# Kernel tuning notes

Hardware: AMD Instinct MI355X
Metric: run time of the kernel (lower is better)

The kernel has to match this reference:

```python
import jax, jax.numpy as jnp
import numpy as np

HEADS = 8
IH, IW = 32, 32
C_IN, C_OUT = 512, 512


def setup_inputs() -> dict:
    key = jax.random.key(0)
    k1, k2, k3, k4, k5 = jax.random.split(key, 5)
    B = 32
    n = IH + IW + (IH // 2) * (IW // 2)  # pooled kv length = 320
    x = jax.random.normal(k1, (B, C_IN, IH, IW), dtype=jnp.float32)
    # 1x1 conv weights stored as [out, in] (bias-free qkv, biased output proj)
    Wqkv = jax.random.normal(k2, (3 * C_IN, C_IN), dtype=jnp.float32) * 0.02
    Wout = jax.random.normal(k3, (C_OUT, C_IN), dtype=jnp.float32) * 0.02
    bout = jnp.zeros((C_OUT,), dtype=jnp.float32)
    pos_embed = jax.random.normal(k4, (1, IH * IW, n), dtype=jnp.float32) * 0.2
    return {"x": x, "Wqkv": Wqkv, "Wout": Wout, "bout": bout, "pos_embed": pos_embed}


def _pool_gate(t, B, C, H, W):
    # adaptive_avg_pool2d(.,(None,1)) == mean over width -> [B,C,H]
    th = t.mean(axis=3)
    # adaptive_avg_pool2d(.,(1,None)) (+permute) == mean over height -> [B,C,W]
    tw = t.mean(axis=2)
    # adaptive_avg_pool2d to (H//2, W//2) with even dims == 2x2 average pooling
    tp = t.reshape(B, C, H // 2, 2, W // 2, 2).mean(axis=(3, 5)).reshape(B, C, -1)
    s = jax.nn.sigmoid(jnp.concatenate([th, tw, tp], axis=2))  # [B,C,n]
    d = C // HEADS
    # 'b (h d) n -> b h n d'
    return s.reshape(B, HEADS, d, -1).transpose(0, 1, 3, 2)


def reference(x, Wqkv, Wout, bout, pos_embed):
    B, C, H, W = x.shape
    d = C // HEADS
    scale = d ** (-0.5)
    qkv = jnp.einsum('bchw,oc->bohw', x, Wqkv)  # 1x1 conv, no bias
    q, k, v = jnp.split(qkv, 3, axis=1)
    # 'b (h d) ih iw -> b h (ih iw) d'
    q = q.reshape(B, HEADS, d, H * W).transpose(0, 1, 3, 2)
    k = _pool_gate(k, B, C, H, W)  # [B,h,n,d]
    v = _pool_gate(v, B, C, H, W)  # [B,h,n,d]
    dots = jnp.einsum('bhsd,bhnd->bhsn', q, k) * scale + pos_embed  # pos_embed [1,s,n] broadcasts
    attn = jax.nn.softmax(dots, axis=-1)
    out = jnp.einsum('bhsn,bhnd->bhsd', attn, v)
    # 'b h (ih iw) d -> b (h d) ih iw'
    out = out.transpose(0, 1, 3, 2).reshape(B, HEADS * d, H, W)
    out = jnp.einsum('bchw,oc->bohw', out, Wout) + bout[None, :, None, None]
    return out
```

## Files before the change

kernel.cpp:

```cpp
#include <hip/hip_runtime.h>
#include <hip/hip_bf16.h>
#include <math.h>

#define HEADS 8
#define CH    512
#define S     1024
#define NKV   320
#define DH    64
#define BATCH 32

typedef __attribute__((ext_vector_type(8))) short short8;
typedef __attribute__((ext_vector_type(4))) short short4v;
typedef __attribute__((ext_vector_type(4))) float float4v;
typedef __attribute__((ext_vector_type(4))) unsigned int uint4v;

__device__ __forceinline__ short f2bf(float f) {
    __hip_bfloat16 h = __float2bfloat16(f);
    return *reinterpret_cast<short*>(&h);
}

__device__ __forceinline__ float fexp2(float x) {
#if __has_builtin(__builtin_amdgcn_exp2f)
    return __builtin_amdgcn_exp2f(x);
#else
    return exp2f(x);
#endif
}

#define GLOAD_LDS16(gp, lp) __builtin_amdgcn_global_load_lds( \
    (const __attribute__((address_space(1))) void*)(gp),      \
    (__attribute__((address_space(3))) void*)(lp), 16, 0, 0)

__global__ __launch_bounds__(256) void pool_kernel2(const float* __restrict__ x,
                                                    short* __restrict__ xpT) {
    __shared__ float sm[4][1024];
    __shared__ short smT[320 * 34];
    const int w = threadIdx.x >> 6;
    const int l = threadIdx.x & 63;
    const int b = blockIdx.y, c0 = blockIdx.x * 32;
    for (int it = 0; it < 8; ++it) {
        const int cix = it * 4 + w;
        const float* src = x + ((size_t)b * 512 + c0 + cix) * 1024;
        #pragma unroll
        for (int j = 0; j < 16; ++j) sm[w][j * 64 + l] = src[j * 64 + l];
        const float* pl = sm[w];
        #pragma unroll
        for (int g = 0; g < 5; ++g) {
            const int nn = g * 64 + l;
            float r;
            if (nn < 32) {
                const int h = nn; float s = 0.f;
                #pragma unroll
                for (int ww = 0; ww < 32; ++ww) s += pl[h * 32 + ww];
                r = s * (1.0f / 32.0f);
            } else if (nn < 64) {
                const int ww = nn - 32; float s = 0.f;
                #pragma unroll
                for (int h = 0; h < 32; ++h) s += pl[h * 32 + ww];
                r = s * (1.0f / 32.0f);
            } else {
                const int i = nn - 64;
                const int ph = i >> 4, pw = i & 15;
                r = 0.25f * (pl[(2 * ph) * 32 + 2 * pw]     + pl[(2 * ph) * 32 + 2 * pw + 1] +
                             pl[(2 * ph + 1) * 32 + 2 * pw] + pl[(2 * ph + 1) * 32 + 2 * pw + 1]);
            }
            smT[nn * 34 + cix] = f2bf(r);
        }
    }
    __syncthreads();
    short* dst = xpT + (size_t)b * NKV * 512 + c0;
    const int r0 = threadIdx.x >> 4, dwi = threadIdx.x & 15;
    #pragma unroll
    for (int pass = 0; pass < 20; ++pass) {
        const int r = pass * 16 + r0;
        const unsigned int v =
            (unsigned int)(unsigned short)smT[r * 34 + dwi * 2] |
            ((unsigned int)(unsigned short)smT[r * 34 + dwi * 2 + 1] << 16);
        *(unsigned int*)&dst[(size_t)r * 512 + dwi * 2] = v;
    }
}

__global__ __launch_bounds__(256) void tcast(const float* __restrict__ in,
                                             short* __restrict__ out, int R, int C) {
    __shared__ float sm[64][65];
    const int t = threadIdx.x;
    const int c0 = blockIdx.x * 64, r0 = blockIdx.y * 64;
    const float* ib = in + ((size_t)blockIdx.z * R + r0) * C + c0;
    #pragma unroll
    for (int rep = 0; rep < 4; ++rep) {
        const int r = rep * 16 + (t >> 4), c = (t & 15) * 4;
        const float4 v = *(const float4*)&ib[(size_t)r * C + c];
        sm[r][c] = v.x; sm[r][c + 1] = v.y; sm[r][c + 2] = v.z; sm[r][c + 3] = v.w;
    }
    __syncthreads();
    short* ob = out + ((size_t)blockIdx.z * C + c0) * R + r0;
    #pragma unroll
    for (int rep = 0; rep < 4; ++rep) {
        const int cr = rep * 16 + (t >> 4), rc = (t & 15) * 4;
        short4v p;
        #pragma unroll
        for (int e = 0; e < 4; ++e) p[e] = f2bf(sm[rc + e][cr]);
        *(short4v*)&ob[(size_t)cr * R + rc] = p;
    }
}

__global__ __launch_bounds__(256) void castw(const float* __restrict__ in,
                                             short* __restrict__ out, int n) {
    const int i = (blockIdx.x * 256 + threadIdx.x) * 4;
    if (i < n) {
        const float4 v = *(const float4*)&in[i];
        short4v p = {f2bf(v.x), f2bf(v.y), f2bf(v.z), f2bf(v.w)};
        *(short4v*)&out[i] = p;
    }
}

template <int MT, int NT, int ACT, typename OT>
__global__ __launch_bounds__(256) void gemm_bf16(const short* __restrict__ A, long sAb,
                                                 const short* __restrict__ B, long sBb,
                                                 const float* __restrict__ bias,
                                                 OT* __restrict__ C, int M, int N) {
    constexpr int K  = 512;
    constexpr int BM = 32 * MT, BN = 32 * NT;
    __shared__ short As[BM * 64];
    __shared__ short Bs[BN * 64];
    const int t = threadIdx.x, w = t >> 6, l = t & 63;
    const int wm = w >> 1, wn = w & 1, quad = l >> 4, m15 = l & 15;
    const int bz = blockIdx.z;
    const int n0 = blockIdx.x * BN, m0 = blockIdx.y * BM;
    const short* gA = A + (size_t)sAb * bz + (size_t)m0 * K;
    const short* gB = B + (size_t)sBb * bz + (size_t)n0 * K;
    const int lrow = l >> 3;
    const int pc   = l & 7;

    const float4v zf = {0.f, 0.f, 0.f, 0.f};
    float4v acc[MT][NT];
    #pragma unroll
    for (int i = 0; i < MT; ++i)
        #pragma unroll
        for (int j = 0; j < NT; ++j) acc[i][j] = zf;

    for (int k0 = 0; k0 < K; k0 += 64) {
        #pragma unroll
        for (int ii = w; ii < BM / 8; ii += 4) {
            const int row = ii * 8 + lrow;
            const int x = pc ^ (row & 7);
            GLOAD_LDS16(gA + (size_t)row * K + k0 + x * 8, &As[ii * 512]);
        }
        #pragma unroll
        for (int ii = w; ii < BN / 8; ii += 4) {
            const int row = ii * 8 + lrow;
            const int x = pc ^ (row & 7);
            GLOAD_LDS16(gB + (size_t)row * K + k0 + x * 8, &Bs[ii * 512]);
        }
        __syncthreads();
        #pragma unroll
        for (int ks = 0; ks < 2; ++ks) {
            const int xa = (((ks * 4 + quad) ^ (m15 & 7))) * 8;
            short8 aF[MT], bF[NT];
            #pragma unroll
            for (int i = 0; i < MT; ++i)
                aF[i] = *(const short8*)&As[((wm * MT + i) * 16 + m15) * 64 + xa];
            #pragma unroll
            for (int j = 0; j < NT; ++j)
                bF[j] = *(const short8*)&Bs[((wn * NT + j) * 16 + m15) * 64 + xa];
            #pragma unroll
            for (int i = 0; i < MT; ++i)
                #pragma unroll
                for (int j = 0; j < NT; ++j)
                    acc[i][j] = __builtin_amdgcn_mfma_f32_16x16x32_bf16(aF[i], bF[j], acc[i][j], 0, 0, 0);
        }
        __syncthreads();
    }

    OT* gC = C + (size_t)bz * M * N;
    #pragma unroll
    for (int i = 0; i < MT; ++i) {
        #pragma unroll
        for (int r = 0; r < 4; ++r) {
            const int row = m0 + (wm * MT + i) * 16 + quad * 4 + r;
            float bv = 0.f;
            if (ACT == 2) bv = bias[row];
            #pragma unroll
            for (int j = 0; j < NT; ++j) {
                const int col = n0 + (wn * NT + j) * 16 + m15;
                float v = acc[i][j][r];
                if (ACT == 1) { v = 1.0f / (1.0f + __expf(-v)); if (col < 512) v *= 0.125f; }
                if (ACT == 2) v += bv;
                if (ACT == 3) v *= 1.4426950408889634f;
                if constexpr (sizeof(OT) == 2)
                    ((short*)gC)[(size_t)row * N + col] = f2bf(v);
                else
                    ((float*)gC)[(size_t)row * N + col] = v;
            }
        }
    }
}

__global__ __launch_bounds__(512, 4) void attn_mfma(const short* __restrict__ qT,
                                                    const short* __restrict__ kvT,
                                                    const float* __restrict__ pos,
                                                    short* __restrict__ aoT) {
    __shared__ short smK[8 * 320 * 8];
    __shared__ short smV[64 * 320];
    const int tid = threadIdx.x, w = tid >> 6, l = tid & 63;
    const int quad = l >> 4, m15 = l & 15;
    const int b = blockIdx.z, h = blockIdx.y, s0 = blockIdx.x * 512;
    const short* kvb = kvT + (size_t)b * NKV * 1024;
    constexpr float LOG2E = 1.4426950408889634f;

    const int nperm = (l & 35) | ((l & 12) << 1) | ((l & 16) >> 2);
    #pragma unroll
    for (int i2 = w; i2 < 40; i2 += 8) {
        const int nb = i2 % 5, dg = i2 / 5;
        GLOAD_LDS16(kvb + (size_t)(nb * 64 + nperm) * 1024 + h * 64 + dg * 8,
                    &smK[(dg * 320 + nb * 64) * 8]);
    }
    #pragma unroll
    for (int it = 0; it < 5; ++it) {
        const int i2 = it * 512 + tid;
        const int n5 = i2 & 31, d8 = (i2 >> 5) & 7, nb = i2 >> 8;
        const int n = nb * 32 + n5;
        const short8 v = *(const short8*)&kvb[(size_t)n * 1024 + 512 + h * 64 + d8 * 8];
        const int x = n >> 3;
        #pragma unroll
        for (int e = 0; e < 8; ++e)
            smV[(d8 * 8 + e) * 320 + ((x ^ e) * 8) + (n & 7)] = v[e];
    }

    __syncthreads();

    const short* qbase = qT + (size_t)(b * S + s0 + w * 16 + m15) * 512 + h * 64;
    const float4v zf = {0.f, 0.f, 0.f, 0.f};

    #pragma unroll 1
    for (int sp = 0; sp < 2; ++sp) {
        asm volatile("" ::: "memory");

        const short* qbA = qbase + (size_t)(2 * sp) * 128 * 512;
        const short* qbB = qbA + (size_t)128 * 512;
        const short8 cqA0 = *(const short8*)&qbA[quad * 8];
        const short8 cqA1 = *(const short8*)&qbA[32 + quad * 8];
        const short8 cqB0 = *(const short8*)&qbB[quad * 8];
        const short8 cqB1 = *(const short8*)&qbB[32 + quad * 8];
        const float* posA = pos + (size_t)(s0 + 2 * sp * 128 + w * 16 + m15) * NKV + quad * 8;
        const float* posB = posA + (size_t)128 * NKV;

        float4v OA0 = zf, OA1 = zf, OA2 = zf, OA3 = zf;
        float4v OB0 = zf, OB1 = zf, OB2 = zf, OB3 = zf;
        float lpA = 0.f, lpB = 0.f;

        #pragma unroll
        for (int c = 0; c < 5; ++c) {
            unsigned int PcA[8], PcB[8];
            #pragma unroll
            for (int t4 = 0; t4 < 4; ++t4) {
                const int tt = c * 4 + t4;
                const short8 k0 = *(const short8*)&smK[(quad * 320 + tt * 16 + m15) * 8];
                const short8 k1 = *(const short8*)&smK[((4 + quad) * 320 + tt * 16 + m15) * 8];
                float4v aA = zf, aB = zf;
                aA = __builtin_amdgcn_mfma_f32_16x16x32_bf16(k0, cqA0, aA, 0, 0, 0);
                aA = __builtin_amdgcn_mfma_f32_16x16x32_bf16(k1, cqA1, aA, 0, 0, 0);
                aB = __builtin_amdgcn_mfma_f32_16x16x32_bf16(k0, cqB0, aB, 0, 0, 0);
                aB = __builtin_amdgcn_mfma_f32_16x16x32_bf16(k1, cqB1, aB, 0, 0, 0);
                const int n0 = c * 64 + (t4 >> 1) * 32 + (t4 & 1) * 4;
                const float4 pvA = *(const float4*)&posA[n0];
                const float4 pvB = *(const float4*)&posB[n0];
                const float a0 = fexp2(fmaf(pvA.x, LOG2E, aA[0]));
                const float a1 = fexp2(fmaf(pvA.y, LOG2E, aA[1]));
                const float a2 = fexp2(fmaf(pvA.z, LOG2E, aA[2]));
                const float a3 = fexp2(fmaf(pvA.w, LOG2E, aA[3]));
                const float b0 = fexp2(fmaf(pvB.x, LOG2E, aB[0]));
                const float b1 = fexp2(fmaf(pvB.y, LOG2E, aB[1]));
                const float b2 = fexp2(fmaf(pvB.z, LOG2E, aB[2]));
                const float b3 = fexp2(fmaf(pvB.w, LOG2E, aB[3]));
                lpA += (a0 + a1) + (a2 + a3);
                lpB += (b0 + b1) + (b2 + b3);
                PcA[t4 * 2]     = (unsigned int)(unsigned short)f2bf(a0) |
                                  ((unsigned int)(unsigned short)f2bf(a1) << 16);
                PcA[t4 * 2 + 1] = (unsigned int)(unsigned short)f2bf(a2) |
                                  ((unsigned int)(unsigned short)f2bf(a3) << 16);
                PcB[t4 * 2]     = (unsigned int)(unsigned short)f2bf(b0) |
                                  ((unsigned int)(unsigned short)f2bf(b1) << 16);
                PcB[t4 * 2 + 1] = (unsigned int)(unsigned short)f2bf(b2) |
                                  ((unsigned int)(unsigned short)f2bf(b3) << 16);
            }
            const uint4v uA0 = {PcA[0], PcA[1], PcA[2], PcA[3]};
            const uint4v uA1 = {PcA[4], PcA[5], PcA[6], PcA[7]};
            const uint4v uB0 = {PcB[0], PcB[1], PcB[2], PcB[3]};
            const uint4v uB1 = {PcB[4], PcB[5], PcB[6], PcB[7]};
            const short8 aPA0 = __builtin_bit_cast(short8, uA0);
            const short8 aPA1 = __builtin_bit_cast(short8, uA1);
            const short8 aPB0 = __builtin_bit_cast(short8, uB0);
            const short8 aPB1 = __builtin_bit_cast(short8, uB1);
            #pragma unroll
            for (int ks = 0; ks < 2; ++ks) {
                const short8 aPA = ks ? aPA1 : aPA0;
                const short8 aPB = ks ? aPB1 : aPB0;
                const int xr = (c * 8 + ks * 4 + quad) ^ (m15 & 7);
                const short8 bV0 = *(const short8*)&smV[(0 * 16 + m15) * 320 + xr * 8];
                const short8 bV1 = *(const short8*)&smV[(1 * 16 + m15) * 320 + xr * 8];
                const short8 bV2 = *(const short8*)&smV[(2 * 16 + m15) * 320 + xr * 8];
                const short8 bV3 = *(const short8*)&smV[(3 * 16 + m15) * 320 + xr * 8];
                OA0 = __builtin_amdgcn_mfma_f32_16x16x32_bf16(aPA, bV0, OA0, 0, 0, 0);
                OB0 = __builtin_amdgcn_mfma_f32_16x16x32_bf16(aPB, bV0, OB0, 0, 0, 0);
                OA1 = __builtin_amdgcn_mfma_f32_16x16x32_bf16(aPA, bV1, OA1, 0, 0, 0);
                OB1 = __builtin_amdgcn_mfma_f32_16x16x32_bf16(aPB, bV1, OB1, 0, 0, 0);
                OA2 = __builtin_amdgcn_mfma_f32_16x16x32_bf16(aPA, bV2, OA2, 0, 0, 0);
                OB2 = __builtin_amdgcn_mfma_f32_16x16x32_bf16(aPB, bV2, OB2, 0, 0, 0);
                OA3 = __builtin_amdgcn_mfma_f32_16x16x32_bf16(aPA, bV3, OA3, 0, 0, 0);
                OB3 = __builtin_amdgcn_mfma_f32_16x16x32_bf16(aPB, bV3, OB3, 0, 0, 0);
            }
        }

        float lrA = lpA, lrB = lpB;
        lrA += __shfl_xor(lrA, 16, 64);
        lrA += __shfl_xor(lrA, 32, 64);
        lrB += __shfl_xor(lrB, 16, 64);
        lrB += __shfl_xor(lrB, 32, 64);
        const float invlA = 1.0f / lrA;
        const float invlB = 1.0f / lrB;
        float invA[4], invB[4];
        #pragma unroll
        for (int r = 0; r < 4; ++r) {
            invA[r] = __shfl(invlA, (l & 48) | (quad * 4 + r), 64);
            invB[r] = __shfl(invlB, (l & 48) | (quad * 4 + r), 64);
        }

        #pragma unroll
        for (int r = 0; r < 4; ++r) {
            const int sA = s0 + 2 * sp * 128 + w * 16 + quad * 4 + r;
            short* orA = &aoT[(size_t)(b * S + sA) * 512 + h * 64 + m15];
            orA[0]  = f2bf(OA0[r] * invA[r]);
            orA[16] = f2bf(OA1[r] * invA[r]);
            orA[32] = f2bf(OA2[r] * invA[r]);
            orA[48] = f2bf(OA3[r] * invA[r]);
            short* orB = orA + (size_t)128 * 512;
            orB[0]  = f2bf(OB0[r] * invB[r]);
            orB[16] = f2bf(OB1[r] * invB[r]);
            orB[32] = f2bf(OB2[r] * invB[r]);
            orB[48] = f2bf(OB3[r] * invB[r]);
        }
    }
}

extern "C" void kernel_launch(void* const* d_in, const int* in_sizes, int n_in,
                              void* d_out, int out_size, void* d_ws, size_t ws_size,
                              hipStream_t stream) {
    const float* x    = (const float*)d_in[0];
    const float* Wqkv = (const float*)d_in[1];
    const float* Wout = (const float*)d_in[2];
    const float* bout = (const float*)d_in[3];
    const float* pos  = (const float*)d_in[4];
    char* ws = (char*)d_ws;
    short* xT   = (short*)(ws + 20971520);
    short* xpT  = (short*)(ws + 54525952);
    short* qT   = (short*)(ws + 65011712);
    short* kvT  = (short*)(ws + 98566144);
    short* aoT  = (short*)(ws + 119537664);
    short* Wbf  = (short*)(ws + 153092096);
    short* Wobf = (short*)(ws + 154664960);
    float* out  = (float*)d_out;

    castw<<<dim3(768), 256, 0, stream>>>(Wqkv, Wbf, 1536 * 512);
    castw<<<dim3(256), 256, 0, stream>>>(Wout, Wobf, 512 * 512);
    pool_kernel2<<<dim3(16, BATCH), 256, 0, stream>>>(x, xpT);
    tcast<<<dim3(16, 8, BATCH), 256, 0, stream>>>(x, xT, CH, S);
    gemm_bf16<4, 4, 3, short><<<dim3(4, 8, BATCH), 256, 0, stream>>>(
        xT, (long)S * CH, Wbf, 0, nullptr, qT, S, CH);
    gemm_bf16<2, 8, 1, short><<<dim3(4, 5, BATCH), 256, 0, stream>>>(
        xpT, (long)NKV * CH, Wbf + CH * CH, 0, nullptr, kvT, NKV, 2 * CH);
    attn_mfma<<<dim3(2, HEADS, BATCH), 512, 0, stream>>>(qT, kvT, pos, aoT);
    gemm_bf16<4, 4, 2, float><<<dim3(8, 4, BATCH), 256, 0, stream>>>(
        Wobf, 0, aoT, (long)S * CH, bout, out, CH, S);
}
```

Measured before the change: 276.9 us.

## Double-buffer GEMM LDS tiles and merge the two weight-cast kernels

The bf16 GEMM now keeps two LDS buffers per operand and issues the global-to-LDS loads for the next K-slice before computing on the current one. This removes one barrier per iteration and overlaps memory latency with the MFMA work. The two weight-cast launches are also merged into one kernel to save a launch. In exchange, LDS use per block doubles, which may lower occupancy for the larger tile configurations.

```diff
diff --git a/kernel.cpp b/kernel.cpp
--- a/kernel.cpp
+++ b/kernel.cpp
@@ -104,13 +104,20 @@
     }
 }
 
-__global__ __launch_bounds__(256) void castw(const float* __restrict__ in,
-                                             short* __restrict__ out, int n) {
+__global__ __launch_bounds__(256) void castw2(const float* __restrict__ a,
+                                              short* __restrict__ oa, int na,
+                                              const float* __restrict__ b,
+                                              short* __restrict__ ob, int nb) {
     const int i = (blockIdx.x * 256 + threadIdx.x) * 4;
-    if (i < n) {
-        const float4 v = *(const float4*)&in[i];
+    if (i < na) {
+        const float4 v = *(const float4*)&a[i];
         short4v p = {f2bf(v.x), f2bf(v.y), f2bf(v.z), f2bf(v.w)};
-        *(short4v*)&out[i] = p;
+        *(short4v*)&oa[i] = p;
+    } else if (i - na < nb) {
+        const int j = i - na;
+        const float4 v = *(const float4*)&b[j];
+        short4v p = {f2bf(v.x), f2bf(v.y), f2bf(v.z), f2bf(v.w)};
+        *(short4v*)&ob[j] = p;
     }
 }
 
@@ -121,8 +128,8 @@
                                                  OT* __restrict__ C, int M, int N) {
     constexpr int K  = 512;
     constexpr int BM = 32 * MT, BN = 32 * NT;
-    __shared__ short As[BM * 64];
-    __shared__ short Bs[BN * 64];
+    __shared__ short As[2][BM * 64];
+    __shared__ short Bs[2][BN * 64];
     const int t = threadIdx.x, w = t >> 6, l = t & 63;
     const int wm = w >> 1, wn = w & 1, quad = l >> 4, m15 = l & 15;
     const int bz = blockIdx.z;
@@ -139,37 +146,43 @@
         #pragma unroll
         for (int j = 0; j < NT; ++j) acc[i][j] = zf;
 
-    for (int k0 = 0; k0 < K; k0 += 64) {
+    auto STAGE = [&](int bf, int k0) {
         #pragma unroll
         for (int ii = w; ii < BM / 8; ii += 4) {
             const int row = ii * 8 + lrow;
             const int x = pc ^ (row & 7);
-            GLOAD_LDS16(gA + (size_t)row * K + k0 + x * 8, &As[ii * 512]);
+            GLOAD_LDS16(gA + (size_t)row * K + k0 + x * 8, &As[bf][ii * 512]);
         }
         #pragma unroll
         for (int ii = w; ii < BN / 8; ii += 4) {
             const int row = ii * 8 + lrow;
             const int x = pc ^ (row & 7);
-            GLOAD_LDS16(gB + (size_t)row * K + k0 + x * 8, &Bs[ii * 512]);
-        }
-        __syncthreads();
+            GLOAD_LDS16(gB + (size_t)row * K + k0 + x * 8, &Bs[bf][ii * 512]);
+        }
+    };
+
+    STAGE(0, 0);
+    __syncthreads();
+    for (int ks8 = 0; ks8 < 8; ++ks8) {
+        const int cur = ks8 & 1;
+        if (ks8 < 7) STAGE(cur ^ 1, (ks8 + 1) * 64);
         #pragma unroll
         for (int ks = 0; ks < 2; ++ks) {
             const int xa = (((ks * 4 + quad) ^ (m15 & 7))) * 8;
             short8 aF[MT], bF[NT];
             #pragma unroll
             for (int i = 0; i < MT; ++i)
-                aF[i] = *(const short8*)&As[((wm * MT + i) * 16 + m15) * 64 + xa];
+                aF[i] = *(const short8*)&As[cur][((wm * MT + i) * 16 + m15) * 64 + xa];
             #pragma unroll
             for (int j = 0; j < NT; ++j)
-                bF[j] = *(const short8*)&Bs[((wn * NT + j) * 16 + m15) * 64 + xa];
+                bF[j] = *(const short8*)&Bs[cur][((wn * NT + j) * 16 + m15) * 64 + xa];
             #pragma unroll
             for (int i = 0; i < MT; ++i)
                 #pragma unroll
                 for (int j = 0; j < NT; ++j)
                     acc[i][j] = __builtin_amdgcn_mfma_f32_16x16x32_bf16(aF[i], bF[j], acc[i][j], 0, 0, 0);
         }
-        __syncthreads();
+        if (ks8 < 7) __syncthreads();
     }
 
     OT* gC = C + (size_t)bz * M * N;
@@ -361,8 +374,7 @@
     short* Wobf = (short*)(ws + 154664960);
     float* out  = (float*)d_out;
 
-    castw<<<dim3(768), 256, 0, stream>>>(Wqkv, Wbf, 1536 * 512);
-    castw<<<dim3(256), 256, 0, stream>>>(Wout, Wobf, 512 * 512);
+    castw2<<<dim3(1024), 256, 0, stream>>>(Wqkv, Wbf, 1536 * 512, Wout, Wobf, 512 * 512);
     pool_kernel2<<<dim3(16, BATCH), 256, 0, stream>>>(x, xpT);
     tcast<<<dim3(16, 8, BATCH), 256, 0, stream>>>(x, xT, CH, S);
     gemm_bf16<4, 4, 3, short><<<dim3(4, 8, BATCH), 256, 0, stream>>>(
```

Result: no change. 274.1 us (-1.0%).
